# Kernel optimization log

Measured on AMD Instinct MI355X. Metric: run time of the kernel, lower is better.

The kernel has to match this reference:

```python
import jax, jax.numpy as jnp
import numpy as np

B, No, Nr, D = 128, 128, 512, 512

def setup_inputs() -> dict:
    key = jax.random.key(0)
    ks = jax.random.split(key, 9)
    s = 1.0 / np.sqrt(2 * D)
    s3 = 1.0 / np.sqrt(3 * D)
    return {
        "obj_vecs": jax.random.normal(ks[0], (B, No, D), jnp.float32),
        "attr_vecs": jax.random.normal(ks[1], (B, No, 2 * D), jnp.float32),
        "rela_vecs": jax.random.normal(ks[2], (B, Nr, D), jnp.float32),
        "edges": jax.random.randint(ks[3], (B, Nr, 2), 0, No, jnp.int64),
        "rela_masks": jnp.ones((B, Nr, 1), jnp.float32),
        "W_att": jax.random.uniform(ks[4], (2 * D, D), jnp.float32, -s, s),
        "b_att": jnp.zeros((D,), jnp.float32),
        "W_attr": jax.random.uniform(ks[5], (2 * D, D), jnp.float32, -s, s),
        "b_attr": jnp.zeros((D,), jnp.float32),
        "W_rela": jax.random.uniform(ks[6], (3 * D, D), jnp.float32, -s3, s3),
        "b_rela": jnp.zeros((D,), jnp.float32),
    }

def reference(obj_vecs, attr_vecs, rela_vecs, edges, rela_masks,
              W_att, b_att, W_attr, b_attr, W_rela, b_rela):
    b, no, d = obj_vecs.shape
    # attr projection: (B,No,2d) -> (B,No,d)
    attr = attr_vecs @ W_att + b_att
    # flatten to 2d with per-batch edge offsets
    obj2 = obj_vecs.reshape(-1, d)
    attr2 = attr.reshape(-1, d)
    rela2 = rela_vecs.reshape(-1, d)
    off = (jnp.arange(b, dtype=edges.dtype) * no)[:, None, None]
    e = (edges + off).reshape(-1, 2)
    # attr branch: cat(obj, attr) -> Linear -> ReLU (+ dropout is identity at eval) + residual
    new_attr = jax.nn.relu(jnp.concatenate([obj2, attr2], -1) @ W_attr + b_attr) + attr2
    # rela branch (rela_gnn_type == 0): cat(s, rela, o)
    s_vecs = obj2[e[:, 0]]
    o_vecs = obj2[e[:, 1]]
    t = jnp.concatenate([s_vecs, rela2, o_vecs], -1)
    new_rela = jax.nn.relu(t @ W_rela + b_rela) + rela2
    new_obj = obj_vecs  # passed through unchanged
    return (new_obj,
            new_attr.reshape(b, no, d),
            new_rela.reshape(b, -1, d) * rela_masks)
```

## Files before the change

kernel.cpp:

```cpp
#include <hip/hip_runtime.h>
#include <hip/hip_bf16.h>
#include <stdint.h>

#define C_B   128
#define C_NO  128
#define C_NR  512
#define C_D   512

typedef __attribute__((ext_vector_type(8))) short  short8;
typedef __attribute__((ext_vector_type(4))) float  floatx4;

__device__ __forceinline__ void load_lds16(const void* g, void* lds) {
  __builtin_amdgcn_global_load_lds(
      (const __attribute__((address_space(1))) void*)g,
      (__attribute__((address_space(3))) void*)lds, 16, 0, 0);
}

__device__ __forceinline__ short bfs(float x) {
  __hip_bfloat16 h = __float2bfloat16(x);
  return *reinterpret_cast<short*>(&h);
}

__global__ void transpose_cvt_k(const float* __restrict__ W,
                                __hip_bfloat16* __restrict__ WT, int K, int N) {
  __shared__ float tile[32][33];
  const int k0 = blockIdx.x * 32;
  const int n0 = blockIdx.y * 32;
  const int tx = threadIdx.x & 31;
  const int ty = threadIdx.x >> 5;
#pragma unroll
  for (int i = ty; i < 32; i += 8)
    tile[i][tx] = W[(size_t)(k0 + i) * N + n0 + tx];
  __syncthreads();
#pragma unroll
  for (int i = ty; i < 32; i += 8)
    WT[(size_t)(n0 + i) * K + k0 + tx] = __float2bfloat16(tile[tx][i]);
}

__global__ void cvt_bf16_k(const float* __restrict__ src,
                           __hip_bfloat16* __restrict__ dst) {
  const size_t i = (size_t)blockIdx.x * blockDim.x + threadIdx.x;
  const float4 f0 = reinterpret_cast<const float4*>(src)[2 * i];
  const float4 f1 = reinterpret_cast<const float4*>(src)[2 * i + 1];
  short8 v;
  v[0] = bfs(f0.x); v[1] = bfs(f0.y); v[2] = bfs(f0.z); v[3] = bfs(f0.w);
  v[4] = bfs(f1.x); v[5] = bfs(f1.y); v[6] = bfs(f1.z); v[7] = bfs(f1.w);
  reinterpret_cast<short8*>(dst)[i] = v;
}

__global__ void copy16_k(const uint4* __restrict__ src, uint4* __restrict__ dst) {
  const size_t i = (size_t)blockIdx.x * blockDim.x + threadIdx.x;
  dst[i] = src[i];
}

template <int MODE, int K>
__global__ __launch_bounds__(256) void gemm_k(
    const __hip_bfloat16* __restrict__ A0,
    const __hip_bfloat16* __restrict__ A1,
    const float* __restrict__ Af32,
    const int* __restrict__ edges,
    const __hip_bfloat16* __restrict__ WT,
    const float* __restrict__ bias,
    const float* __restrict__ resid,
    const float* __restrict__ mask,
    float* __restrict__ Cout,
    __hip_bfloat16* __restrict__ CoutBf) {
  constexpr int BK = 32;
  __shared__ __align__(16) __hip_bfloat16 As[128 * BK];
  __shared__ __align__(16) __hip_bfloat16 Bs[128 * BK];

  const int t = threadIdx.x;
  const int lane = t & 63;
  const int w = t >> 6;
  const int m0 = blockIdx.y * 128;
  const int n0 = blockIdx.x * 128;

  const int aRow = t >> 2;
  const int aCol = (t & 3) * 8;

  int sr0 = 0, sr1 = 0, or0 = 0, or1 = 0;
  if constexpr (MODE == 2) {
    const int r0 = m0 + aRow;
    const int r1 = r0 + 64;
    sr0 = (r0 >> 9) * C_NO + edges[2 * r0];
    or0 = (r0 >> 9) * C_NO + edges[2 * r0 + 1];
    sr1 = (r1 >> 9) * C_NO + edges[2 * r1];
    or1 = (r1 >> 9) * C_NO + edges[2 * r1 + 1];
  }

  floatx4 acc[4][4];
#pragma unroll
  for (int i = 0; i < 4; ++i)
#pragma unroll
    for (int j = 0; j < 4; ++j) acc[i][j] = (floatx4)0.0f;

  const int wm = (w >> 1) * 64;
  const int wn = (w & 1) * 64;
  const int fm = lane & 15;
  const int kq = (lane >> 4) * 8;

  for (int kt = 0; kt < K; kt += BK) {
#pragma unroll
    for (int j = 0; j < 2; ++j)
      load_lds16(WT + (size_t)(n0 + j * 64 + aRow) * K + kt + aCol,
                 &Bs[j * 2048 + w * 512]);
#pragma unroll
    for (int j = 0; j < 2; ++j) {
      const int kg = kt + aCol;
      if constexpr (MODE == 0) {
        load_lds16(A0 + (size_t)(m0 + j * 64 + aRow) * K + kg,
                   &As[j * 2048 + w * 512]);
      } else if constexpr (MODE == 1) {
        const __hip_bfloat16* s =
            (kg < C_D) ? A0 + (size_t)(m0 + j * 64 + aRow) * C_D + kg
                       : A1 + (size_t)(m0 + j * 64 + aRow) * C_D + (kg - C_D);
        load_lds16(s, &As[j * 2048 + w * 512]);
      } else {
        const int region = kg >> 9;
        if (region == 1) {
          const float* srcA = Af32 + (size_t)(m0 + j * 64 + aRow) * C_D + (kg - C_D);
          const float4 f0 = *reinterpret_cast<const float4*>(srcA);
          const float4 f1 = *reinterpret_cast<const float4*>(srcA + 4);
          short8 v;
          v[0] = bfs(f0.x); v[1] = bfs(f0.y); v[2] = bfs(f0.z); v[3] = bfs(f0.w);
          v[4] = bfs(f1.x); v[5] = bfs(f1.y); v[6] = bfs(f1.z); v[7] = bfs(f1.w);
          *reinterpret_cast<short8*>(&As[j * 2048 + t * 8]) = v;
        } else {
          const int row = (region == 0) ? (j ? sr1 : sr0) : (j ? or1 : or0);
          const int col = (region == 0) ? kg : (kg - 2 * C_D);
          load_lds16(A0 + (size_t)row * C_D + col, &As[j * 2048 + w * 512]);
        }
      }
    }
    __syncthreads();

    short8 af[4], bf[4];
#pragma unroll
    for (int mi = 0; mi < 4; ++mi)
      af[mi] = *reinterpret_cast<const short8*>(&As[(wm + mi * 16 + fm) * BK + kq]);
#pragma unroll
    for (int ni = 0; ni < 4; ++ni)
      bf[ni] = *reinterpret_cast<const short8*>(&Bs[(wn + ni * 16 + fm) * BK + kq]);
#pragma unroll
    for (int mi = 0; mi < 4; ++mi)
#pragma unroll
      for (int ni = 0; ni < 4; ++ni)
        acc[mi][ni] =
            __builtin_amdgcn_mfma_f32_16x16x32_bf16(af[mi], bf[ni], acc[mi][ni], 0, 0, 0);
    __syncthreads();
  }

  float bv[4];
#pragma unroll
  for (int ni = 0; ni < 4; ++ni)
    bv[ni] = bias[n0 + wn + ni * 16 + fm];

#pragma unroll
  for (int mi = 0; mi < 4; ++mi) {
    const int rb = m0 + wm + mi * 16 + (lane >> 4) * 4;
#pragma unroll
    for (int i = 0; i < 4; ++i) {
      const int cm = rb + i;
      float mv = 1.0f;
      if constexpr (MODE == 2) mv = mask[cm];
#pragma unroll
      for (int ni = 0; ni < 4; ++ni) {
        const int cn = n0 + wn + ni * 16 + fm;
        float v = acc[mi][ni][i] + bv[ni];
        if constexpr (MODE == 0) {
          Cout[(size_t)cm * C_D + cn] = v;
          CoutBf[(size_t)cm * C_D + cn] = __float2bfloat16(v);
        } else {
          v = fmaxf(v, 0.0f) + resid[(size_t)cm * C_D + cn];
          if constexpr (MODE == 2) v *= mv;
          Cout[(size_t)cm * C_D + cn] = v;
        }
      }
    }
  }
}

extern "C" void kernel_launch(void* const* d_in, const int* in_sizes, int n_in,
                              void* d_out, int out_size, void* d_ws, size_t ws_size,
                              hipStream_t stream) {
  const float* obj       = (const float*)d_in[0];
  const float* attr_vecs = (const float*)d_in[1];
  const float* rela      = (const float*)d_in[2];
  const int*   edges     = (const int*)d_in[3];
  const float* masks     = (const float*)d_in[4];
  const float* W_att     = (const float*)d_in[5];
  const float* b_att     = (const float*)d_in[6];
  const float* W_attr    = (const float*)d_in[7];
  const float* b_attr    = (const float*)d_in[8];
  const float* W_rela    = (const float*)d_in[9];
  const float* b_rela    = (const float*)d_in[10];

  float* out      = (float*)d_out;
  float* out_obj  = out;
  float* out_attr = out + 8388608;
  float* out_rela = out + 16777216;

  __hip_bfloat16* obj_bf   = (__hip_bfloat16*)out_obj;
  __hip_bfloat16* WT_rela  = (__hip_bfloat16*)(out_obj + 4194304);
  __hip_bfloat16* attr_bf  = (__hip_bfloat16*)out_rela;
  __hip_bfloat16* attrS_bf = (__hip_bfloat16*)(out_rela + 8388608);
  __hip_bfloat16* WT_attr  = (__hip_bfloat16*)(out_rela + 33030144);
  __hip_bfloat16* WT_att   = (__hip_bfloat16*)(out_rela + 33292288);
  float*          attrS    = out_attr;

  transpose_cvt_k<<<dim3(32, 16), 256, 0, stream>>>(W_att, WT_att, 1024, 512);
  transpose_cvt_k<<<dim3(32, 16), 256, 0, stream>>>(W_attr, WT_attr, 1024, 512);
  transpose_cvt_k<<<dim3(48, 16), 256, 0, stream>>>(W_rela, WT_rela, 1536, 512);

  cvt_bf16_k<<<4096, 256, 0, stream>>>(obj, obj_bf);
  cvt_bf16_k<<<8192, 256, 0, stream>>>(attr_vecs, attr_bf);

  gemm_k<0, 1024><<<dim3(4, 128), 256, 0, stream>>>(
      attr_bf, nullptr, nullptr, nullptr, WT_att, b_att, nullptr, nullptr,
      attrS, attrS_bf);

  gemm_k<1, 1024><<<dim3(4, 128), 256, 0, stream>>>(
      obj_bf, attrS_bf, nullptr, nullptr, WT_attr, b_attr, attrS, nullptr,
      out_attr, nullptr);

  gemm_k<2, 1536><<<dim3(4, 512), 256, 0, stream>>>(
      obj_bf, nullptr, rela, edges, WT_rela, b_rela, rela, masks,
      out_rela, nullptr);

  copy16_k<<<8192, 256, 0, stream>>>((const uint4*)obj, (uint4*)out_obj);
}
```

Baseline: 660.2 us.

## Double-buffer GEMM LDS tiles, swizzle block order, fuse attr fp32-to-bf16 conversion

The GEMM kernel now double-buffers its LDS tiles, issuing global loads for the next K step before running the MFMAs on the current one, so memory latency overlaps compute. The first GEMM reads fp32 attr_vecs directly and converts them to bf16 inside the kernel, which removes a separate conversion pass and its extra round trip through memory. Workgroup indices are remapped across eight groups to change the launch order, and launch bounds request four blocks per CU. The costs are doubled LDS use and more register pressure from the prefetch registers, which could limit occupancy.

After: 560.7 us. 1.18x faster.

```diff
diff --git a/kernel.cpp b/kernel.cpp
--- a/kernel.cpp
+++ b/kernel.cpp
@@ -54,7 +54,7 @@
 }
 
 template <int MODE, int K>
-__global__ __launch_bounds__(256) void gemm_k(
+__global__ __launch_bounds__(256, 4) void gemm_k(
     const __hip_bfloat16* __restrict__ A0,
     const __hip_bfloat16* __restrict__ A1,
     const float* __restrict__ Af32,
@@ -66,14 +66,18 @@
     float* __restrict__ Cout,
     __hip_bfloat16* __restrict__ CoutBf) {
   constexpr int BK = 32;
-  __shared__ __align__(16) __hip_bfloat16 As[128 * BK];
-  __shared__ __align__(16) __hip_bfloat16 Bs[128 * BK];
+  __shared__ __align__(16) __hip_bfloat16 As[2][128 * BK];
+  __shared__ __align__(16) __hip_bfloat16 Bs[2][128 * BK];
 
   const int t = threadIdx.x;
   const int lane = t & 63;
   const int w = t >> 6;
-  const int m0 = blockIdx.y * 128;
-  const int n0 = blockIdx.x * 128;
+
+  const int nwg = gridDim.x * gridDim.y;
+  const int flat = blockIdx.y * gridDim.x + blockIdx.x;
+  const int lb = (flat & 7) * (nwg >> 3) + (flat >> 3);
+  const int n0 = (lb & 3) * 128;
+  const int m0 = (lb >> 2) * 128;
 
   const int aRow = t >> 2;
   const int aCol = (t & 3) * 8;
@@ -99,54 +103,96 @@
   const int fm = lane & 15;
   const int kq = (lane >> 4) * 8;
 
-  for (int kt = 0; kt < K; kt += BK) {
+  float4 pa[2], pb[2];
+  int pend = 0;
+
+  auto stage_issue = [&](int p, int kt) {
+    const int kg = kt + aCol;
+    if constexpr (MODE == 0) {
+      const float* s0 = Af32 + (size_t)(m0 + aRow) * K + kg;
+      const float* s1 = Af32 + (size_t)(m0 + 64 + aRow) * K + kg;
+      pa[0] = *reinterpret_cast<const float4*>(s0);
+      pb[0] = *reinterpret_cast<const float4*>(s0 + 4);
+      pa[1] = *reinterpret_cast<const float4*>(s1);
+      pb[1] = *reinterpret_cast<const float4*>(s1 + 4);
+      pend = 1;
+    } else if constexpr (MODE == 2) {
+      if ((kg >> 9) == 1) {
+        const float* s0 = Af32 + (size_t)(m0 + aRow) * C_D + (kg - C_D);
+        const float* s1 = Af32 + (size_t)(m0 + 64 + aRow) * C_D + (kg - C_D);
+        pa[0] = *reinterpret_cast<const float4*>(s0);
+        pb[0] = *reinterpret_cast<const float4*>(s0 + 4);
+        pa[1] = *reinterpret_cast<const float4*>(s1);
+        pb[1] = *reinterpret_cast<const float4*>(s1 + 4);
+        pend = 1;
+      }
+    }
 #pragma unroll
     for (int j = 0; j < 2; ++j)
       load_lds16(WT + (size_t)(n0 + j * 64 + aRow) * K + kt + aCol,
-                 &Bs[j * 2048 + w * 512]);
-#pragma unroll
-    for (int j = 0; j < 2; ++j) {
-      const int kg = kt + aCol;
-      if constexpr (MODE == 0) {
-        load_lds16(A0 + (size_t)(m0 + j * 64 + aRow) * K + kg,
-                   &As[j * 2048 + w * 512]);
-      } else if constexpr (MODE == 1) {
+                 &Bs[p][j * 2048 + w * 512]);
+    if constexpr (MODE == 1) {
+#pragma unroll
+      for (int j = 0; j < 2; ++j) {
         const __hip_bfloat16* s =
             (kg < C_D) ? A0 + (size_t)(m0 + j * 64 + aRow) * C_D + kg
                        : A1 + (size_t)(m0 + j * 64 + aRow) * C_D + (kg - C_D);
-        load_lds16(s, &As[j * 2048 + w * 512]);
-      } else {
-        const int region = kg >> 9;
-        if (region == 1) {
-          const float* srcA = Af32 + (size_t)(m0 + j * 64 + aRow) * C_D + (kg - C_D);
-          const float4 f0 = *reinterpret_cast<const float4*>(srcA);
-          const float4 f1 = *reinterpret_cast<const float4*>(srcA + 4);
-          short8 v;
-          v[0] = bfs(f0.x); v[1] = bfs(f0.y); v[2] = bfs(f0.z); v[3] = bfs(f0.w);
-          v[4] = bfs(f1.x); v[5] = bfs(f1.y); v[6] = bfs(f1.z); v[7] = bfs(f1.w);
-          *reinterpret_cast<short8*>(&As[j * 2048 + t * 8]) = v;
-        } else {
+        load_lds16(s, &As[p][j * 2048 + w * 512]);
+      }
+    } else if constexpr (MODE == 2) {
+      const int region = kg >> 9;
+      if (region != 1) {
+#pragma unroll
+        for (int j = 0; j < 2; ++j) {
           const int row = (region == 0) ? (j ? sr1 : sr0) : (j ? or1 : or0);
           const int col = (region == 0) ? kg : (kg - 2 * C_D);
-          load_lds16(A0 + (size_t)row * C_D + col, &As[j * 2048 + w * 512]);
+          load_lds16(A0 + (size_t)row * C_D + col, &As[p][j * 2048 + w * 512]);
         }
       }
     }
-    __syncthreads();
-
-    short8 af[4], bf[4];
+  };
+
+  auto stage_finish = [&](int p) {
+    if constexpr (MODE != 1) {
+      if (pend) {
+#pragma unroll
+        for (int j = 0; j < 2; ++j) {
+          short8 v;
+          v[0] = bfs(pa[j].x); v[1] = bfs(pa[j].y);
+          v[2] = bfs(pa[j].z); v[3] = bfs(pa[j].w);
+          v[4] = bfs(pb[j].x); v[5] = bfs(pb[j].y);
+          v[6] = bfs(pb[j].z); v[7] = bfs(pb[j].w);
+          *reinterpret_cast<short8*>(&As[p][j * 2048 + t * 8]) = v;
+        }
+        pend = 0;
+      }
+    }
+  };
+
+  stage_issue(0, 0);
+  stage_finish(0);
+  __syncthreads();
+
+  int p = 0;
+  for (int kt = 0; kt < K; kt += BK, p ^= 1) {
+    const bool more = (kt + BK) < K;
+    if (more) stage_issue(p ^ 1, kt + BK);
+
+    short8 af[4], br[4];
 #pragma unroll
     for (int mi = 0; mi < 4; ++mi)
-      af[mi] = *reinterpret_cast<const short8*>(&As[(wm + mi * 16 + fm) * BK + kq]);
+      af[mi] = *reinterpret_cast<const short8*>(&As[p][(wm + mi * 16 + fm) * BK + kq]);
 #pragma unroll
     for (int ni = 0; ni < 4; ++ni)
-      bf[ni] = *reinterpret_cast<const short8*>(&Bs[(wn + ni * 16 + fm) * BK + kq]);
+      br[ni] = *reinterpret_cast<const short8*>(&Bs[p][(wn + ni * 16 + fm) * BK + kq]);
 #pragma unroll
     for (int mi = 0; mi < 4; ++mi)
 #pragma unroll
       for (int ni = 0; ni < 4; ++ni)
         acc[mi][ni] =
-            __builtin_amdgcn_mfma_f32_16x16x32_bf16(af[mi], bf[ni], acc[mi][ni], 0, 0, 0);
+            __builtin_amdgcn_mfma_f32_16x16x32_bf16(af[mi], br[ni], acc[mi][ni], 0, 0, 0);
+
+    if (more) stage_finish(p ^ 1);
     __syncthreads();
   }
 
@@ -202,8 +248,7 @@
 
   __hip_bfloat16* obj_bf   = (__hip_bfloat16*)out_obj;
   __hip_bfloat16* WT_rela  = (__hip_bfloat16*)(out_obj + 4194304);
-  __hip_bfloat16* attr_bf  = (__hip_bfloat16*)out_rela;
-  __hip_bfloat16* attrS_bf = (__hip_bfloat16*)(out_rela + 8388608);
+  __hip_bfloat16* attrS_bf = (__hip_bfloat16*)out_rela;
   __hip_bfloat16* WT_attr  = (__hip_bfloat16*)(out_rela + 33030144);
   __hip_bfloat16* WT_att   = (__hip_bfloat16*)(out_rela + 33292288);
   float*          attrS    = out_attr;
@@ -213,10 +258,9 @@
   transpose_cvt_k<<<dim3(48, 16), 256, 0, stream>>>(W_rela, WT_rela, 1536, 512);
 
   cvt_bf16_k<<<4096, 256, 0, stream>>>(obj, obj_bf);
-  cvt_bf16_k<<<8192, 256, 0, stream>>>(attr_vecs, attr_bf);
 
   gemm_k<0, 1024><<<dim3(4, 128), 256, 0, stream>>>(
-      attr_bf, nullptr, nullptr, nullptr, WT_att, b_att, nullptr, nullptr,
+      nullptr, nullptr, attr_vecs, nullptr, WT_att, b_att, nullptr, nullptr,
       attrS, attrS_bf);
 
   gemm_k<1, 1024><<<dim3(4, 128), 256, 0, stream>>>(
```
